# Kernel tuning notes

Hardware: AMD Instinct MI355X
Metric: run time of the kernel (lower is better)

Reference implementation:

```python
import jax, jax.numpy as jnp
import numpy as np


def setup_inputs() -> dict:
    key = jax.random.key(0)
    ks = jax.random.split(key, 5)
    B, H, W, C = 64, 14, 14, 2048
    x = jax.random.normal(ks[0], (B, H, W, C), dtype=jnp.float32)
    # Glorot-ish scaled 1x1 conv weights (stored as [Cin, Cout])
    W1 = jax.random.normal(ks[1], (C, 64), dtype=jnp.float32) * (1.0 / np.sqrt(C))
    W2 = jax.random.normal(ks[2], (64, 16), dtype=jnp.float32) * (1.0 / np.sqrt(64))
    W3 = jax.random.normal(ks[3], (16, 8), dtype=jnp.float32) * (1.0 / np.sqrt(16))
    W4 = jax.random.normal(ks[4], (8, 1), dtype=jnp.float32) * (1.0 / np.sqrt(8))
    return {
        "x": x,
        "W1": W1, "b1": jnp.zeros((64,), jnp.float32),
        "W2": W2, "b2": jnp.zeros((16,), jnp.float32),
        "W3": W3, "b3": jnp.zeros((8,), jnp.float32),
        "W4": W4, "b4": jnp.zeros((1,), jnp.float32),
    }


def reference(x, W1, b1, W2, b2, W3, b3, W4, b4):
    # Dropout is identity at inference time.
    # 1x1 convs == per-pixel matmuls over channel dim.
    h = jax.nn.relu(jnp.einsum('bhwc,cd->bhwd', x, W1) + b1)   # [B,H,W,64]
    h = jax.nn.relu(jnp.einsum('bhwc,cd->bhwd', h, W2) + b2)   # [B,H,W,16]
    h = jax.nn.relu(jnp.einsum('bhwc,cd->bhwd', h, W3) + b3)   # [B,H,W,8]
    a = jax.nn.sigmoid(jnp.einsum('bhwc,cd->bhwd', h, W4) + b4)  # [B,H,W,1]
    # 'upsample' frozen ones-conv == broadcast of a over 2048 channels.
    gap_features = jnp.mean(a * x, axis=(1, 2))  # [B, 2048]
    gap_mask = jnp.mean(a, axis=(1, 2))          # [B, 1] (same value for all 2048 chans)
    return gap_features / gap_mask               # [B, 2048]
```

## Files before the change

### kernel.cpp

```cpp
#include <hip/hip_runtime.h>
#include <math.h>

#define NPIX 12544
#define CIN  2048
#define NB   64
#define PPIX 196

typedef short  bf16x8 __attribute__((ext_vector_type(8)));
typedef float  f32x4  __attribute__((ext_vector_type(4)));

__device__ inline unsigned short f2bf(float f) {
    unsigned int u = __float_as_uint(f);
    u = (u + 0x7fffu + ((u >> 16) & 1u)) >> 16;
    return (unsigned short)u;
}

__global__ __launch_bounds__(256) void conv_w1(
    const float* __restrict__ W1, unsigned short* __restrict__ W1t)
{
    const int id = blockIdx.x * 256 + threadIdx.x;
    const int n = id >> 11;
    const int k = id & 2047;
    W1t[id] = f2bf(W1[k * 64 + n]);
}

__global__ __launch_bounds__(64) void attn_scores_mfma(
    const float* __restrict__ x, const unsigned short* __restrict__ W1t,
    const float* __restrict__ b1,
    const float* __restrict__ W2, const float* __restrict__ b2,
    const float* __restrict__ W3, const float* __restrict__ b3,
    const float* __restrict__ W4, const float* __restrict__ b4,
    float* __restrict__ a_out)
{
    __shared__ float h1s[16][68];

    const int lane = threadIdx.x;
    const int l15  = lane & 15;
    const int q    = lane >> 4;
    const size_t pix0 = (size_t)blockIdx.x * 16;

    const float* xr = x + (pix0 + l15) * (size_t)CIN + q * 8;
    const unsigned short* wr = W1t + (size_t)l15 * CIN + q * 8;

    f32x4 acc[4] = {{0,0,0,0},{0,0,0,0},{0,0,0,0},{0,0,0,0}};

#pragma unroll 2
    for (int k0 = 0; k0 < CIN; k0 += 32) {
        float4 xa = *(const float4*)(xr + k0);
        float4 xb = *(const float4*)(xr + k0 + 4);
        bf16x8 af;
        af[0] = (short)f2bf(xa.x); af[1] = (short)f2bf(xa.y);
        af[2] = (short)f2bf(xa.z); af[3] = (short)f2bf(xa.w);
        af[4] = (short)f2bf(xb.x); af[5] = (short)f2bf(xb.y);
        af[6] = (short)f2bf(xb.z); af[7] = (short)f2bf(xb.w);
#pragma unroll
        for (int ct = 0; ct < 4; ++ct) {
            bf16x8 bfr = *(const bf16x8*)(wr + (size_t)ct * 16 * CIN + k0);
            acc[ct] = __builtin_amdgcn_mfma_f32_16x16x32_bf16(af, bfr, acc[ct], 0, 0, 0);
        }
    }

#pragma unroll
    for (int ct = 0; ct < 4; ++ct) {
        const float bias = b1[ct * 16 + l15];
#pragma unroll
        for (int r = 0; r < 4; ++r)
            h1s[q * 4 + r][ct * 16 + l15] = fmaxf(acc[ct][r] + bias, 0.f);
    }
    __syncthreads();

    if (lane < 16) {
        float hv[64];
#pragma unroll
        for (int i = 0; i < 16; ++i) {
            float4 t = *(const float4*)&h1s[lane][i * 4];
            hv[i*4+0] = t.x; hv[i*4+1] = t.y; hv[i*4+2] = t.z; hv[i*4+3] = t.w;
        }
        float h2[16];
#pragma unroll
        for (int j = 0; j < 16; ++j) {
            float s = b2[j];
#pragma unroll
            for (int k = 0; k < 64; ++k) s = fmaf(hv[k], W2[k * 16 + j], s);
            h2[j] = fmaxf(s, 0.f);
        }
        float h3[8];
#pragma unroll
        for (int j = 0; j < 8; ++j) {
            float s = b3[j];
#pragma unroll
            for (int k = 0; k < 16; ++k) s = fmaf(h2[k], W3[k * 8 + j], s);
            h3[j] = fmaxf(s, 0.f);
        }
        float z = b4[0];
#pragma unroll
        for (int k = 0; k < 8; ++k) z = fmaf(h3[k], W4[k], z);
        a_out[pix0 + lane] = 1.f / (1.f + expf(-z));
    }
}

__global__ __launch_bounds__(256) void gap_partial(
    const float* __restrict__ x, const float* __restrict__ a,
    float* __restrict__ part)
{
    const int b  = blockIdx.y;
    const int pz = blockIdx.z;
    const int c0 = (blockIdx.x * 256 + threadIdx.x) * 4;
    const float* xb = x + ((size_t)b * PPIX + pz * 98) * CIN + c0;
    const float* ab = a + b * PPIX + pz * 98;

    float4 s0 = {0,0,0,0}, s1 = {0,0,0,0};
#pragma unroll 4
    for (int p = 0; p < 98; p += 2) {
        const float a0 = ab[p], a1 = ab[p + 1];
        const float4 v0 = *(const float4*)(xb + (size_t)p * CIN);
        const float4 v1 = *(const float4*)(xb + (size_t)(p + 1) * CIN);
        s0.x = fmaf(a0, v0.x, s0.x); s0.y = fmaf(a0, v0.y, s0.y);
        s0.z = fmaf(a0, v0.z, s0.z); s0.w = fmaf(a0, v0.w, s0.w);
        s1.x = fmaf(a1, v1.x, s1.x); s1.y = fmaf(a1, v1.y, s1.y);
        s1.z = fmaf(a1, v1.z, s1.z); s1.w = fmaf(a1, v1.w, s1.w);
    }
    float4 r;
    r.x = s0.x + s1.x; r.y = s0.y + s1.y; r.z = s0.z + s1.z; r.w = s0.w + s1.w;
    *(float4*)(part + ((size_t)pz * NB + b) * CIN + c0) = r;
}

__global__ __launch_bounds__(512) void gap_final(
    const float* __restrict__ a, const float* __restrict__ part,
    float* __restrict__ out)
{
    __shared__ float red[512];
    const int b = blockIdx.x, t = threadIdx.x;
    red[t] = (t < PPIX) ? a[b * PPIX + t] : 0.f;
    __syncthreads();
#pragma unroll
    for (int s = 256; s > 0; s >>= 1) {
        if (t < s) red[t] += red[t + s];
        __syncthreads();
    }
    const float inv = 1.f / red[0];
    const int c0 = t * 4;
    const float4 p0 = *(const float4*)(part + ((size_t)0 * NB + b) * CIN + c0);
    const float4 p1 = *(const float4*)(part + ((size_t)1 * NB + b) * CIN + c0);
    float4 r;
    r.x = (p0.x + p1.x) * inv; r.y = (p0.y + p1.y) * inv;
    r.z = (p0.z + p1.z) * inv; r.w = (p0.w + p1.w) * inv;
    *(float4*)(out + (size_t)b * CIN + c0) = r;
}

extern "C" void kernel_launch(void* const* d_in, const int* in_sizes, int n_in,
                              void* d_out, int out_size, void* d_ws, size_t ws_size,
                              hipStream_t stream)
{
    const float* x  = (const float*)d_in[0];
    const float* W1 = (const float*)d_in[1];
    const float* b1 = (const float*)d_in[2];
    const float* W2 = (const float*)d_in[3];
    const float* b2 = (const float*)d_in[4];
    const float* W3 = (const float*)d_in[5];
    const float* b3 = (const float*)d_in[6];
    const float* W4 = (const float*)d_in[7];
    const float* b4 = (const float*)d_in[8];
    float* out = (float*)d_out;

    unsigned short* W1t = (unsigned short*)d_ws;
    float* a    = (float*)((char*)d_ws + (256 << 10));
    float* part = (float*)((char*)d_ws + (512 << 10));

    conv_w1<<<512, 256, 0, stream>>>(W1, W1t);
    attn_scores_mfma<<<NPIX / 16, 64, 0, stream>>>(x, W1t, b1, W2, b2, W3, b3, W4, b4, a);
    gap_partial<<<dim3(2, NB, 2), 256, 0, stream>>>(x, a, part);
    gap_final<<<NB, 512, 0, stream>>>(a, part, out);
}
```

Before: 201.0 us.

## Split attention GEMM K across 8 waves and widen GAP pixel split

The attention-score kernel now runs 512 threads per 16-pixel block. Each of its 8 waves computes a 256-wide K slice with MFMA, and the partial sums are reduced through shared memory. The small MLP tail is spread across 256 threads per layer instead of running serially in 16 lanes. The GAP partial kernel splits pixels into 7 chunks instead of 2, giving 896 blocks instead of 256 to fill the GPU, and the final kernel sums the 7 partials. The cost is more shared memory, extra syncs and a larger partial buffer.

```diff
diff --git a/kernel.cpp b/kernel.cpp
--- a/kernel.cpp
+++ b/kernel.cpp
@@ -5,6 +5,8 @@
 #define CIN  2048
 #define NB   64
 #define PPIX 196
+#define PSPLIT 7
+#define PCHUNK 28
 
 typedef short  bf16x8 __attribute__((ext_vector_type(8)));
 typedef float  f32x4  __attribute__((ext_vector_type(4)));
@@ -24,7 +26,7 @@
     W1t[id] = f2bf(W1[k * 64 + n]);
 }
 
-__global__ __launch_bounds__(64) void attn_scores_mfma(
+__global__ __launch_bounds__(512) void attn_scores_mfma(
     const float* __restrict__ x, const unsigned short* __restrict__ W1t,
     const float* __restrict__ b1,
     const float* __restrict__ W2, const float* __restrict__ b2,
@@ -32,20 +34,25 @@
     const float* __restrict__ W4, const float* __restrict__ b4,
     float* __restrict__ a_out)
 {
+    __shared__ float part[8][16][68];
     __shared__ float h1s[16][68];
+    __shared__ float h2s[16][16];
+    __shared__ float h3s[16][8];
 
-    const int lane = threadIdx.x;
+    const int t    = threadIdx.x;
+    const int wv   = t >> 6;
+    const int lane = t & 63;
     const int l15  = lane & 15;
     const int q    = lane >> 4;
     const size_t pix0 = (size_t)blockIdx.x * 16;
 
-    const float* xr = x + (pix0 + l15) * (size_t)CIN + q * 8;
-    const unsigned short* wr = W1t + (size_t)l15 * CIN + q * 8;
+    const float* xr = x + (pix0 + l15) * (size_t)CIN + wv * 256 + q * 8;
+    const unsigned short* wr = W1t + (size_t)l15 * CIN + wv * 256 + q * 8;
 
     f32x4 acc[4] = {{0,0,0,0},{0,0,0,0},{0,0,0,0},{0,0,0,0}};
 
 #pragma unroll 2
-    for (int k0 = 0; k0 < CIN; k0 += 32) {
+    for (int k0 = 0; k0 < 256; k0 += 32) {
         float4 xa = *(const float4*)(xr + k0);
         float4 xb = *(const float4*)(xr + k0 + 4);
         bf16x8 af;
@@ -61,41 +68,49 @@
     }
 
 #pragma unroll
-    for (int ct = 0; ct < 4; ++ct) {
-        const float bias = b1[ct * 16 + l15];
+    for (int ct = 0; ct < 4; ++ct)
 #pragma unroll
         for (int r = 0; r < 4; ++r)
-            h1s[q * 4 + r][ct * 16 + l15] = fmaxf(acc[ct][r] + bias, 0.f);
+            part[wv][q * 4 + r][ct * 16 + l15] = acc[ct][r];
+    __syncthreads();
+
+    const int p = t >> 4;
+    const int j = t & 15;
+
+    if (t < 256) {
+        const int c0 = j * 4;
+        f32x4 s = {0, 0, 0, 0};
+#pragma unroll
+        for (int w = 0; w < 8; ++w) s += *(const f32x4*)&part[w][p][c0];
+        const f32x4 bb = *(const f32x4*)(b1 + c0);
+        f32x4 hv;
+#pragma unroll
+        for (int i = 0; i < 4; ++i) hv[i] = fmaxf(s[i] + bb[i], 0.f);
+        *(f32x4*)&h1s[p][c0] = hv;
     }
     __syncthreads();
 
-    if (lane < 16) {
-        float hv[64];
+    if (t < 256) {
+        float s = b2[j];
 #pragma unroll
-        for (int i = 0; i < 16; ++i) {
-            float4 t = *(const float4*)&h1s[lane][i * 4];
-            hv[i*4+0] = t.x; hv[i*4+1] = t.y; hv[i*4+2] = t.z; hv[i*4+3] = t.w;
-        }
-        float h2[16];
+        for (int k = 0; k < 64; ++k) s = fmaf(h1s[p][k], W2[k * 16 + j], s);
+        h2s[p][j] = fmaxf(s, 0.f);
+    }
+    __syncthreads();
+
+    if (t < 256 && j < 8) {
+        float s = b3[j];
 #pragma unroll
-        for (int j = 0; j < 16; ++j) {
-            float s = b2[j];
-#pragma unroll
-            for (int k = 0; k < 64; ++k) s = fmaf(hv[k], W2[k * 16 + j], s);
-            h2[j] = fmaxf(s, 0.f);
-        }
-        float h3[8];
-#pragma unroll
-        for (int j = 0; j < 8; ++j) {
-            float s = b3[j];
-#pragma unroll
-            for (int k = 0; k < 16; ++k) s = fmaf(h2[k], W3[k * 8 + j], s);
-            h3[j] = fmaxf(s, 0.f);
-        }
+        for (int k = 0; k < 16; ++k) s = fmaf(h2s[p][k], W3[k * 8 + j], s);
+        h3s[p][j] = fmaxf(s, 0.f);
+    }
+    __syncthreads();
+
+    if (t < 256 && j == 0) {
         float z = b4[0];
 #pragma unroll
-        for (int k = 0; k < 8; ++k) z = fmaf(h3[k], W4[k], z);
-        a_out[pix0 + lane] = 1.f / (1.f + expf(-z));
+        for (int k = 0; k < 8; ++k) z = fmaf(h3s[p][k], W4[k], z);
+        a_out[pix0 + p] = 1.f / (1.f + expf(-z));
     }
 }
 
@@ -106,12 +121,12 @@
     const int b  = blockIdx.y;
     const int pz = blockIdx.z;
     const int c0 = (blockIdx.x * 256 + threadIdx.x) * 4;
-    const float* xb = x + ((size_t)b * PPIX + pz * 98) * CIN + c0;
-    const float* ab = a + b * PPIX + pz * 98;
+    const float* xb = x + ((size_t)b * PPIX + pz * PCHUNK) * CIN + c0;
+    const float* ab = a + b * PPIX + pz * PCHUNK;
 
     float4 s0 = {0,0,0,0}, s1 = {0,0,0,0};
 #pragma unroll 4
-    for (int p = 0; p < 98; p += 2) {
+    for (int p = 0; p < PCHUNK; p += 2) {
         const float a0 = ab[p], a1 = ab[p + 1];
         const float4 v0 = *(const float4*)(xb + (size_t)p * CIN);
         const float4 v1 = *(const float4*)(xb + (size_t)(p + 1) * CIN);
@@ -140,11 +155,14 @@
     }
     const float inv = 1.f / red[0];
     const int c0 = t * 4;
-    const float4 p0 = *(const float4*)(part + ((size_t)0 * NB + b) * CIN + c0);
-    const float4 p1 = *(const float4*)(part + ((size_t)1 * NB + b) * CIN + c0);
+    float4 acc = {0, 0, 0, 0};
+#pragma unroll
+    for (int z = 0; z < PSPLIT; ++z) {
+        const float4 pv = *(const float4*)(part + ((size_t)z * NB + b) * CIN + c0);
+        acc.x += pv.x; acc.y += pv.y; acc.z += pv.z; acc.w += pv.w;
+    }
     float4 r;
-    r.x = (p0.x + p1.x) * inv; r.y = (p0.y + p1.y) * inv;
-    r.z = (p0.z + p1.z) * inv; r.w = (p0.w + p1.w) * inv;
+    r.x = acc.x * inv; r.y = acc.y * inv; r.z = acc.z * inv; r.w = acc.w * inv;
     *(float4*)(out + (size_t)b * CIN + c0) = r;
 }
 
@@ -168,7 +186,7 @@
     float* part = (float*)((char*)d_ws + (512 << 10));
 
     conv_w1<<<512, 256, 0, stream>>>(W1, W1t);
-    attn_scores_mfma<<<NPIX / 16, 64, 0, stream>>>(x, W1t, b1, W2, b2, W3, b3, W4, b4, a);
-    gap_partial<<<dim3(2, NB, 2), 256, 0, stream>>>(x, a, part);
+    attn_scores_mfma<<<NPIX / 16, 512, 0, stream>>>(x, W1t, b1, W2, b2, W3, b3, W4, b4, a);
+    gap_partial<<<dim3(2, NB, PSPLIT), 256, 0, stream>>>(x, a, part);
     gap_final<<<NB, 512, 0, stream>>>(a, part, out);
 }
```

Measured after the change: 213.8 us. +6.4%, slower.

## Replace bf16 MFMA first layer with split-K fp32 GEMV and parallel MLP tail

Applied to the files above, without the earlier changes.

Computes the first 1x1 conv as an fp32 FMA GEMV split eight ways along channels, with W1 slices staged into LDS via direct global-to-LDS loads and x prefetched per pixel. Partial sums are written to a workspace and reduced in a separate tail kernel that spreads the small MLP layers across 256 threads. The aim is more parallelism and memory-level concurrency than the small-block MFMA kernel, and it drops the weight conversion kernel and bf16 rounding. In exchange it adds a large partial-sum buffer round trip and one more launch dependency.

```diff
diff --git a/kernel.cpp b/kernel.cpp
--- a/kernel.cpp
+++ b/kernel.cpp
@@ -1,101 +1,120 @@
 #include <hip/hip_runtime.h>
 #include <math.h>
 
-#define NPIX 12544
 #define CIN  2048
 #define NB   64
 #define PPIX 196
+#define NPIX 12544
+#define KZN  8
+#define KSL  256
+#define PXB  56
+#define PXW  7
+#define NPB  (NPIX / PXB)
 
-typedef short  bf16x8 __attribute__((ext_vector_type(8)));
-typedef float  f32x4  __attribute__((ext_vector_type(4)));
+typedef float f32x4 __attribute__((ext_vector_type(4)));
 
-__device__ inline unsigned short f2bf(float f) {
-    unsigned int u = __float_as_uint(f);
-    u = (u + 0x7fffu + ((u >> 16) & 1u)) >> 16;
-    return (unsigned short)u;
+__global__ __launch_bounds__(512, 4) void h1_gemv(
+    const float* __restrict__ x, const float* __restrict__ W1,
+    float* __restrict__ h1part)
+{
+    __shared__ float Wl[KSL * 64];
+    const int t    = threadIdx.x;
+    const int wv   = t >> 6;
+    const int lane = t & 63;
+    const int pb   = blockIdx.x;
+    const int kz   = blockIdx.y;
+
+    {
+        const char* wsrc = (const char*)(W1 + (size_t)kz * KSL * 64);
+        char* wdst = (char*)Wl;
+#pragma unroll
+        for (int j = 0; j < 8; ++j)
+            __builtin_amdgcn_global_load_lds(
+                (const float*)(wsrc + (wv * 8 + j) * 1024 + lane * 16),
+                (float*)(wdst + (wv * 8 + j) * 1024), 16, 0, 0);
+    }
+    __syncthreads();
+
+    const int pix0 = pb * PXB + wv * PXW;
+    const float* xr0 = x + (size_t)pix0 * CIN + kz * KSL;
+
+    float acc[PXW];
+#pragma unroll
+    for (int p = 0; p < PXW; ++p) acc[p] = 0.f;
+
+    f32x4 xc[PXW], xn[PXW];
+#pragma unroll
+    for (int p = 0; p < PXW; ++p) xc[p] = *(const f32x4*)(xr0 + (size_t)p * CIN);
+#pragma unroll
+    for (int p = 0; p < PXW; ++p) xn[p] = xc[p];
+
+    for (int kb = 0; kb < KSL / 4; ++kb) {
+        if (kb < KSL / 4 - 1) {
+#pragma unroll
+            for (int p = 0; p < PXW; ++p)
+                xn[p] = *(const f32x4*)(xr0 + (size_t)p * CIN + (kb + 1) * 4);
+        }
+        const int k0 = kb * 4;
+        const float w0 = Wl[(k0 + 0) * 64 + lane];
+        const float w1 = Wl[(k0 + 1) * 64 + lane];
+        const float w2 = Wl[(k0 + 2) * 64 + lane];
+        const float w3 = Wl[(k0 + 3) * 64 + lane];
+#pragma unroll
+        for (int p = 0; p < PXW; ++p)
+            acc[p] = fmaf(xc[p][3], w3, fmaf(xc[p][2], w2,
+                     fmaf(xc[p][1], w1, fmaf(xc[p][0], w0, acc[p]))));
+#pragma unroll
+        for (int p = 0; p < PXW; ++p) xc[p] = xn[p];
+    }
+#pragma unroll
+    for (int p = 0; p < PXW; ++p)
+        h1part[((size_t)kz * NPIX + pix0 + p) * 64 + lane] = acc[p];
 }
 
-__global__ __launch_bounds__(256) void conv_w1(
-    const float* __restrict__ W1, unsigned short* __restrict__ W1t)
-{
-    const int id = blockIdx.x * 256 + threadIdx.x;
-    const int n = id >> 11;
-    const int k = id & 2047;
-    W1t[id] = f2bf(W1[k * 64 + n]);
-}
-
-__global__ __launch_bounds__(64) void attn_scores_mfma(
-    const float* __restrict__ x, const unsigned short* __restrict__ W1t,
-    const float* __restrict__ b1,
+__global__ __launch_bounds__(256) void attn_tail(
+    const float* __restrict__ h1part, const float* __restrict__ b1,
     const float* __restrict__ W2, const float* __restrict__ b2,
     const float* __restrict__ W3, const float* __restrict__ b3,
     const float* __restrict__ W4, const float* __restrict__ b4,
     float* __restrict__ a_out)
 {
-    __shared__ float h1s[16][68];
+    __shared__ float h1s[16][72];
+    __shared__ float h2s[16][16];
+    __shared__ float h3s[16][8];
+    const int t = threadIdx.x, blk = blockIdx.x;
+    const int p = t >> 4, j = t & 15;
+    const int pix = blk * 16 + p;
 
-    const int lane = threadIdx.x;
-    const int l15  = lane & 15;
-    const int q    = lane >> 4;
-    const size_t pix0 = (size_t)blockIdx.x * 16;
+    f32x4 s = *(const f32x4*)(b1 + j * 4);
+#pragma unroll
+    for (int kz = 0; kz < KZN; ++kz)
+        s += *(const f32x4*)(h1part + ((size_t)kz * NPIX + pix) * 64 + j * 4);
+    f32x4 hv;
+#pragma unroll
+    for (int i = 0; i < 4; ++i) hv[i] = fmaxf(s[i], 0.f);
+    *(f32x4*)&h1s[p][j * 4] = hv;
+    __syncthreads();
 
-    const float* xr = x + (pix0 + l15) * (size_t)CIN + q * 8;
-    const unsigned short* wr = W1t + (size_t)l15 * CIN + q * 8;
-
-    f32x4 acc[4] = {{0,0,0,0},{0,0,0,0},{0,0,0,0},{0,0,0,0}};
-
-#pragma unroll 2
-    for (int k0 = 0; k0 < CIN; k0 += 32) {
-        float4 xa = *(const float4*)(xr + k0);
-        float4 xb = *(const float4*)(xr + k0 + 4);
-        bf16x8 af;
-        af[0] = (short)f2bf(xa.x); af[1] = (short)f2bf(xa.y);
-        af[2] = (short)f2bf(xa.z); af[3] = (short)f2bf(xa.w);
-        af[4] = (short)f2bf(xb.x); af[5] = (short)f2bf(xb.y);
-        af[6] = (short)f2bf(xb.z); af[7] = (short)f2bf(xb.w);
+    {
+        float v = b2[j];
 #pragma unroll
-        for (int ct = 0; ct < 4; ++ct) {
-            bf16x8 bfr = *(const bf16x8*)(wr + (size_t)ct * 16 * CIN + k0);
-            acc[ct] = __builtin_amdgcn_mfma_f32_16x16x32_bf16(af, bfr, acc[ct], 0, 0, 0);
-        }
-    }
-
-#pragma unroll
-    for (int ct = 0; ct < 4; ++ct) {
-        const float bias = b1[ct * 16 + l15];
-#pragma unroll
-        for (int r = 0; r < 4; ++r)
-            h1s[q * 4 + r][ct * 16 + l15] = fmaxf(acc[ct][r] + bias, 0.f);
+        for (int k = 0; k < 64; ++k) v = fmaf(h1s[p][k], W2[k * 16 + j], v);
+        h2s[p][j] = fmaxf(v, 0.f);
     }
     __syncthreads();
-
-    if (lane < 16) {
-        float hv[64];
+    if (t < 128) {
+        const int p3 = t >> 3, j3 = t & 7;
+        float v = b3[j3];
 #pragma unroll
-        for (int i = 0; i < 16; ++i) {
-            float4 t = *(const float4*)&h1s[lane][i * 4];
-            hv[i*4+0] = t.x; hv[i*4+1] = t.y; hv[i*4+2] = t.z; hv[i*4+3] = t.w;
-        }
-        float h2[16];
-#pragma unroll
-        for (int j = 0; j < 16; ++j) {
-            float s = b2[j];
-#pragma unroll
-            for (int k = 0; k < 64; ++k) s = fmaf(hv[k], W2[k * 16 + j], s);
-            h2[j] = fmaxf(s, 0.f);
-        }
-        float h3[8];
-#pragma unroll
-        for (int j = 0; j < 8; ++j) {
-            float s = b3[j];
-#pragma unroll
-            for (int k = 0; k < 16; ++k) s = fmaf(h2[k], W3[k * 8 + j], s);
-            h3[j] = fmaxf(s, 0.f);
-        }
+        for (int k = 0; k < 16; ++k) v = fmaf(h2s[p3][k], W3[k * 8 + j3], v);
+        h3s[p3][j3] = fmaxf(v, 0.f);
+    }
+    __syncthreads();
+    if (t < 16) {
         float z = b4[0];
 #pragma unroll
-        for (int k = 0; k < 8; ++k) z = fmaf(h3[k], W4[k], z);
-        a_out[pix0 + lane] = 1.f / (1.f + expf(-z));
+        for (int k = 0; k < 8; ++k) z = fmaf(h3s[t][k], W4[k], z);
+        a_out[blk * 16 + t] = 1.f / (1.f + expf(-z));
     }
 }
 
@@ -109,7 +128,7 @@
     const float* xb = x + ((size_t)b * PPIX + pz * 98) * CIN + c0;
     const float* ab = a + b * PPIX + pz * 98;
 
-    float4 s0 = {0,0,0,0}, s1 = {0,0,0,0};
+    float4 s0 = {0, 0, 0, 0}, s1 = {0, 0, 0, 0};
 #pragma unroll 4
     for (int p = 0; p < 98; p += 2) {
         const float a0 = ab[p], a1 = ab[p + 1];
@@ -163,12 +182,12 @@
     const float* b4 = (const float*)d_in[8];
     float* out = (float*)d_out;
 
-    unsigned short* W1t = (unsigned short*)d_ws;
-    float* a    = (float*)((char*)d_ws + (256 << 10));
-    float* part = (float*)((char*)d_ws + (512 << 10));
+    float* a      = (float*)((char*)d_ws + (256 << 10));
+    float* h1part = (float*)((char*)d_ws + (1 << 20));
+    float* part   = (float*)((char*)d_ws + (28u << 20));
 
-    conv_w1<<<512, 256, 0, stream>>>(W1, W1t);
-    attn_scores_mfma<<<NPIX / 16, 64, 0, stream>>>(x, W1t, b1, W2, b2, W3, b3, W4, b4, a);
+    h1_gemv<<<dim3(NPB, KZN), 512, 0, stream>>>(x, W1, h1part);
+    attn_tail<<<NPIX / 16, 256, 0, stream>>>(h1part, b1, W2, b2, W3, b3, W4, b4, a);
     gap_partial<<<dim3(2, NB, 2), 256, 0, stream>>>(x, a, part);
     gap_final<<<NB, 512, 0, stream>>>(a, part, out);
 }
```

Measured after the change: 374.0 us. 1.86x slower.
